# Performance work log

Measured on AMD Instinct MI355X. Metric: run time of the kernel, lower is better.

Reference implementation:

```python
import jax, jax.numpy as jnp
import numpy as np

B, S, D = 2, 2048, 2048
H, HD = 16, 128
ROPE_THETA = 10000.0


def _rope_cos_sin(seq_len, head_dim, dtype=jnp.float32):
    inv_freq = 1.0 / (ROPE_THETA ** (jnp.arange(0, head_dim, 2, dtype=jnp.float32) / head_dim))
    t = jnp.arange(seq_len, dtype=jnp.float32)
    freqs = jnp.outer(t, inv_freq)                     # [S, HD/2]
    emb = jnp.concatenate([freqs, freqs], axis=-1)     # [S, HD]
    return jnp.cos(emb).astype(dtype), jnp.sin(emb).astype(dtype)


def _rotate_half(x):
    x1, x2 = jnp.split(x, 2, axis=-1)
    return jnp.concatenate([-x2, x1], axis=-1)


def _apply_rope(x, cos, sin):
    # x: [B, S, H, HD]; cos/sin: [S, HD] -> broadcast over batch and heads
    c = cos[None, :, None, :]
    s = sin[None, :, None, :]
    return x * c + _rotate_half(x) * s


def setup_inputs() -> dict:
    key = jax.random.key(0)
    ks = jax.random.split(key, 6)
    scale = 1.0 / np.sqrt(D)
    hidden_states = jax.random.normal(ks[0], (B, S, D), dtype=jnp.float32)
    # causal additive mask: 0 on/below diagonal, large negative above
    neg = jnp.finfo(jnp.float32).min
    causal = jnp.where(jnp.tril(jnp.ones((S, S), dtype=bool)), 0.0, neg)
    attention_mask = jnp.broadcast_to(causal[None, None, :, :], (B, 1, S, S)).astype(jnp.float32)
    Wq = jax.random.normal(ks[1], (D, D), dtype=jnp.float32) * scale
    Wk = jax.random.normal(ks[2], (D, D), dtype=jnp.float32) * scale
    Wv = jax.random.normal(ks[3], (D, D), dtype=jnp.float32) * scale
    Wo = jax.random.normal(ks[4], (D, D), dtype=jnp.float32) * scale
    return {"hidden_states": hidden_states, "attention_mask": attention_mask,
            "Wq": Wq, "Wk": Wk, "Wv": Wv, "Wo": Wo}


def reference(hidden_states, attention_mask, Wq, Wk, Wv, Wo):
    b, s, d = hidden_states.shape
    # projections (torch Linear: x @ W^T)
    q = (hidden_states @ Wq.T).reshape(b, s, H, HD)
    k = (hidden_states @ Wk.T).reshape(b, s, H, HD)
    v = (hidden_states @ Wv.T).reshape(b, s, H, HD)
    cos, sin = _rope_cos_sin(s, HD, hidden_states.dtype)
    q = _apply_rope(q, cos, sin)
    k = _apply_rope(k, cos, sin)
    # naive attention, [B, H, S, S] scores materialized as in the original
    scores = jnp.einsum('bqhd,bkhd->bhqk', q, k) / np.sqrt(HD)
    scores = scores + attention_mask
    attn = jax.nn.softmax(scores, axis=-1)
    out = jnp.einsum('bhqk,bkhd->bqhd', attn, v).reshape(b, s, d)
    return out @ Wo.T
```

## Files before the change

### kernel.cpp

```cpp
#include <hip/hip_runtime.h>
#include <hip/hip_bf16.h>

typedef __hip_bfloat16 bf16;
typedef __attribute__((ext_vector_type(8))) short s16x8;
typedef __attribute__((ext_vector_type(4))) float f32x4;
typedef __attribute__((ext_vector_type(16))) float f32x16;

#define MFMA16(a, b, c) __builtin_amdgcn_mfma_f32_16x16x32_bf16(a, b, c, 0, 0, 0)
#define MFMA32(a, b, c) __builtin_amdgcn_mfma_f32_32x32x16_bf16(a, b, c, 0, 0, 0)

#define GLL16(gsrc, ldst)                                                                 \
  __builtin_amdgcn_global_load_lds(                                                       \
      (const __attribute__((address_space(1))) unsigned int*)(gsrc),                      \
      (__attribute__((address_space(3))) unsigned int*)(ldst), 16, 0, 0)

#define VMCNT(n) asm volatile("s_waitcnt vmcnt(" #n ")" ::: "memory")
#define BARRIER() __builtin_amdgcn_s_barrier()

static constexpr int S_LEN = 2048;
static constexpr int D_DIM = 2048;
static constexpr int NY = 6144;

union BF4 { ushort4 u; bf16 b[4]; };

__device__ inline unsigned pack2(float a, float b) {
  union { bf16 h[2]; unsigned u; } x;
  x.h[0] = __float2bfloat16(a);
  x.h[1] = __float2bfloat16(b);
  return x.u;
}

__global__ void convert_all(const float* __restrict__ X, const float* __restrict__ Wq,
                            const float* __restrict__ Wk, const float* __restrict__ Wv,
                            const float* __restrict__ Wo, bf16* __restrict__ Xb,
                            bf16* __restrict__ Wb, bf16* __restrict__ Wob,
                            float* __restrict__ cosT, float* __restrict__ sinT) {
  int gid = blockIdx.x * 256 + threadIdx.x;
  if (gid < 6291456) {
    int i4 = gid * 4;
    const float* src;
    bf16* dst;
    int off;
    if (i4 < 8388608) {
      src = X; dst = Xb; off = i4;
    } else {
      int j = i4 - 8388608;
      int seg = j >> 22;
      off = j & 4194303;
      if (seg == 0) { src = Wq; dst = Wb; }
      else if (seg == 1) { src = Wk; dst = Wb + 4194304; }
      else if (seg == 2) { src = Wv; dst = Wb + 8388608; }
      else { src = Wo; dst = Wob; }
    }
    float4 v = *(const float4*)(src + off);
    BF4 o;
    o.b[0] = __float2bfloat16(v.x);
    o.b[1] = __float2bfloat16(v.y);
    o.b[2] = __float2bfloat16(v.z);
    o.b[3] = __float2bfloat16(v.w);
    *(ushort4*)(dst + off) = o.u;
  } else {
    int t4 = (gid - 6291456) * 4;
    if (t4 < 131072) {
#pragma unroll
      for (int k = 0; k < 4; ++k) {
        int i = t4 + k;
        int d = i & 63, s = i >> 6;
        float inv = powf(10000.0f, -(float)d * (1.0f / 64.0f));
        float ang = (float)s * inv;
        cosT[i] = cosf(ang);
        sinT[i] = sinf(ang);
      }
    }
  }
}

__global__ __launch_bounds__(256) void rope_qk(bf16* __restrict__ Y,
                                               const float* __restrict__ cosT,
                                               const float* __restrict__ sinT) {
  int idx = blockIdx.x * 256 + threadIdx.x;
  int quad = idx & 15;
  int h = (idx >> 4) & 15;
  int m = (idx >> 8) & 4095;
  int g = idx >> 20;
  int s = m & (S_LEN - 1);
  int d0 = quad * 4;
  float sc = g ? 1.0f : 0.08838834764831845f * 1.4426950408889634f;
  bf16* p = Y + (size_t)m * NY + g * D_DIM + h * 128 + d0;
  BF4 lo, hi, olo, ohi;
  lo.u = *(const ushort4*)p;
  hi.u = *(const ushort4*)(p + 64);
  float4 c = *(const float4*)(cosT + s * 64 + d0);
  float4 sn = *(const float4*)(sinT + s * 64 + d0);
  float cc[4] = {c.x, c.y, c.z, c.w};
  float ss[4] = {sn.x, sn.y, sn.z, sn.w};
#pragma unroll
  for (int i = 0; i < 4; ++i) {
    float x1 = __bfloat162float(lo.b[i]);
    float x2 = __bfloat162float(hi.b[i]);
    olo.b[i] = __float2bfloat16((x1 * cc[i] - x2 * ss[i]) * sc);
    ohi.b[i] = __float2bfloat16((x2 * cc[i] + x1 * ss[i]) * sc);
  }
  *(ushort4*)p = olo.u;
  *(ushort4*)(p + 64) = ohi.u;
}

__device__ inline void storeC(float* p, float v) { *p = v; }
__device__ inline void storeC(bf16* p, float v) { *p = __float2bfloat16(v); }

__global__ __launch_bounds__(512, 2) void gemm256(const bf16* __restrict__ A,
                                                  const bf16* __restrict__ Bm,
                                                  bf16* __restrict__ C, int K, int lda,
                                                  int ldb, int ldc, int mt) {
  __shared__ __align__(16) char lds[131072];
  char* A0buf = lds;
  char* B0buf = lds + 32768;
  char* A1buf = lds + 65536;
  char* B1buf = lds + 98304;
  const int tid = threadIdx.x;
  const int lane = tid & 63;
  const int w = tid >> 6;
  const int wm = w >> 2, wn = w & 3;
  const int l15 = lane & 15, lh4 = lane >> 4;
  const int xr = l15 & 7;
  const int xo0 = ((lh4 ^ xr) << 4);
  const int xo1 = (((4 + lh4) ^ xr) << 4);

  const int nwg = gridDim.x;
  const int bid = blockIdx.x;
  const int swz = (bid & 7) * (nwg >> 3) + (bid >> 3);
  const int bm = swz % mt, bn = swz / mt;
  const int row0 = bm * 256, col0 = bn * 256;

  const int srow8 = lane >> 3;
  const int scol = ((lane & 7) ^ srow8) * 8;
  const bf16* gA_s = A + (size_t)(row0 + w * 8 + srow8) * lda + scol;
  const bf16* gB_s = Bm + (size_t)(col0 + (w >> 2) * 64 + (w & 3) * 8 + srow8) * ldb + scol;
  const int ldst = w * 1024;

#define STAGE_A(bufa, rh, k0)                                                     \
  {                                                                               \
    GLL16(gA_s + (size_t)((rh)*64) * lda + (k0), (bufa) + (rh)*16384 + ldst);     \
    GLL16(gA_s + (size_t)((rh)*64 + 128) * lda + (k0),                            \
          (bufa) + (rh)*16384 + 8192 + ldst);                                     \
  }
#define STAGE_B(bufb, ch, k0)                                                     \
  {                                                                               \
    GLL16(gB_s + (size_t)((ch)*32) * ldb + (k0), (bufb) + (ch)*16384 + ldst);     \
    GLL16(gB_s + (size_t)((ch)*32 + 128) * ldb + (k0),                            \
          (bufb) + (ch)*16384 + 8192 + ldst);                                     \
  }

  f32x4 acc[8][4];
#pragma unroll
  for (int i = 0; i < 8; ++i)
#pragma unroll
    for (int j = 0; j < 4; ++j) acc[i][j] = (f32x4){0.f, 0.f, 0.f, 0.f};

  s16x8 af[4][2];
  s16x8 bfr[2][2];

#define READ_AH(bufa, rh)                                                         \
  _Pragma("unroll") for (int ii = 0; ii < 4; ++ii) {                              \
    const char* p_ = (bufa) + (rh)*16384 + (wm * 64 + ii * 16 + l15) * 128;       \
    af[ii][0] = *(const s16x8*)(p_ + xo0);                                        \
    af[ii][1] = *(const s16x8*)(p_ + xo1);                                        \
  }
#define READ_BH(bufb, ch)                                                         \
  _Pragma("unroll") for (int jj = 0; jj < 2; ++jj) {                              \
    const char* p_ = (bufb) + (ch)*16384 + (wn * 32 + jj * 16 + l15) * 128;       \
    bfr[jj][0] = *(const s16x8*)(p_ + xo0);                                       \
    bfr[jj][1] = *(const s16x8*)(p_ + xo1);                                       \
  }
#define QUAD(rh, ch)                                                              \
  __builtin_amdgcn_s_setprio(1);                                                  \
  _Pragma("unroll") for (int jj = 0; jj < 2; ++jj)                                \
  _Pragma("unroll") for (int ii = 0; ii < 4; ++ii)                                \
  _Pragma("unroll") for (int ks = 0; ks < 2; ++ks)                                \
      acc[(rh)*4 + ii][(ch)*2 + jj] =                                             \
          MFMA16(af[ii][ks], bfr[jj][ks], acc[(rh)*4 + ii][(ch)*2 + jj]);         \
  __builtin_amdgcn_s_setprio(0);

  STAGE_A(A0buf, 0, 0);
  STAGE_B(B0buf, 0, 0);
  STAGE_B(B0buf, 1, 0);
  STAGE_A(A0buf, 1, 0);
  STAGE_A(A1buf, 0, 64);
  STAGE_B(B1buf, 1, 64);
  STAGE_A(A1buf, 1, 64);
  VMCNT(6);
  BARRIER();

  const int NI = K >> 7;
  for (int i = 0; i < NI; ++i) {
    const int kT1 = (2 * i + 1) << 6;
    const int kT2 = (2 * i + 2) << 6;
    const int kT3 = (2 * i + 3) << 6;
    const bool nl = (i + 1 < NI);
    READ_AH(A0buf, 0);
    READ_BH(B0buf, 0);
    STAGE_B(B1buf, 0, kT1);
    BARRIER();
    QUAD(0, 0);
    BARRIER();
    READ_BH(B0buf, 1);
    if (nl) STAGE_A(A0buf, 0, kT2);
    BARRIER();
    QUAD(0, 1);
    BARRIER();
    READ_AH(A0buf, 1);
    if (nl) STAGE_B(B0buf, 1, kT2);
    BARRIER();
    QUAD(1, 1);
    BARRIER();
    READ_BH(B0buf, 0);
    if (nl) STAGE_A(A0buf, 1, kT2);
    BARRIER();
    QUAD(1, 0);
    if (nl) { VMCNT(6); } else { VMCNT(0); }
    BARRIER();
    READ_AH(A1buf, 0);
    READ_BH(B1buf, 0);
    if (nl) STAGE_B(B0buf, 0, kT2);
    BARRIER();
    QUAD(0, 0);
    BARRIER();
    READ_BH(B1buf, 1);
    if (nl) STAGE_A(A1buf, 0, kT3);
    BARRIER();
    QUAD(0, 1);
    BARRIER();
    READ_AH(A1buf, 1);
    if (nl) STAGE_B(B1buf, 1, kT3);
    BARRIER();
    QUAD(1, 1);
    BARRIER();
    READ_BH(B1buf, 0);
    if (nl) STAGE_A(A1buf, 1, kT3);
    BARRIER();
    QUAD(1, 0);
    if (nl) { VMCNT(6); }
    BARRIER();
  }
#undef STAGE_A
#undef STAGE_B
#undef READ_AH
#undef READ_BH
#undef QUAD

#pragma unroll
  for (int ri = 0; ri < 8; ++ri)
#pragma unroll
    for (int cj = 0; cj < 4; ++cj) {
      int gr = row0 + wm * 128 + ri * 16 + lh4 * 4;
      int gc = col0 + wn * 64 + cj * 16 + l15;
#pragma unroll
      for (int rr = 0; rr < 4; ++rr)
        C[(size_t)(gr + rr) * ldc + gc] = __float2bfloat16(acc[ri][cj][rr]);
    }
}

template <typename OutT, bool TRANSV>
__global__ __launch_bounds__(512, 2) void gemm_fine(const bf16* __restrict__ A,
                                                    const bf16* __restrict__ Bm,
                                                    OutT* __restrict__ C, int K, int lda,
                                                    int ldb, int ldc, int mt) {
  __shared__ __align__(16) char lds[147456];
  char* b0 = lds;
  char* b1 = lds + 49152;
  char* b2 = lds + 98304;
  const int tid = threadIdx.x;
  const int lane = tid & 63;
  const int w = tid >> 6;
  const int wm = w >> 2, wn = w & 3;
  const int l15 = lane & 15, lh4 = lane >> 4;
  const int xr = l15 & 7;
  const int xo0 = ((lh4 ^ xr) << 4);
  const int xo1 = (((4 + lh4) ^ xr) << 4);

  const int nwg = gridDim.x;
  const int bid = blockIdx.x;
  const int swz = (bid & 7) * (nwg >> 3) + (bid >> 3);
  const int bm = swz % mt, bn = swz / mt;
  const int row0 = bm * 128, col0 = bn * 256;

  const int srow = w * 8 + (lane >> 3);
  const int scol = ((lane & 7) ^ (lane >> 3)) * 8;
  const bf16* gA = A + (size_t)(row0 + srow) * lda + scol;
  const bf16* gB = Bm + (size_t)(col0 + srow) * ldb + scol;
  const int ldst = w * 1024;

  f32x4 acc[4][4];
#pragma unroll
  for (int i = 0; i < 4; ++i)
#pragma unroll
    for (int j = 0; j < 4; ++j) acc[i][j] = (f32x4){0.f, 0.f, 0.f, 0.f};

  s16x8 af[4], bfr[4];

#define PH_READ(BUF, XO)                                                          \
  _Pragma("unroll") for (int ii = 0; ii < 4; ++ii)                                \
      af[ii] = *(const s16x8*)((BUF) + (wm * 64 + ii * 16 + l15) * 128 + (XO));   \
  _Pragma("unroll") for (int jj = 0; jj < 4; ++jj)                                \
      bfr[jj] = *(const s16x8*)((BUF) + 16384 + (wn * 64 + jj * 16 + l15) * 128 + (XO));
#define PH_FMA()                                                                  \
  __builtin_amdgcn_s_setprio(1);                                                  \
  _Pragma("unroll") for (int jj = 0; jj < 4; ++jj)                                \
  _Pragma("unroll") for (int ii = 0; ii < 4; ++ii)                                \
      acc[ii][jj] = MFMA16(af[ii], bfr[jj], acc[ii][jj]);                         \
  __builtin_amdgcn_s_setprio(0);
#define STAGE_T(BUF, kS)                                                          \
  GLL16(gA + (kS), (BUF) + ldst);                                                 \
  GLL16(gA + (size_t)64 * lda + (kS), (BUF) + 8192 + ldst);                       \
  GLL16(gB + (kS), (BUF) + 16384 + ldst);                                         \
  GLL16(gB + (size_t)64 * ldb + (kS), (BUF) + 24576 + ldst);                      \
  GLL16(gB + (size_t)128 * ldb + (kS), (BUF) + 32768 + ldst);                     \
  GLL16(gB + (size_t)192 * ldb + (kS), (BUF) + 40960 + ldst);
#define TILE_MAIN(RBUF, SBUF, kS)                                                 \
  PH_READ(RBUF, xo0);                                                             \
  GLL16(gA + (kS), (SBUF) + ldst);                                                \
  GLL16(gA + (size_t)64 * lda + (kS), (SBUF) + 8192 + ldst);                      \
  GLL16(gB + (kS), (SBUF) + 16384 + ldst);                                        \
  BARRIER();                                                                      \
  PH_FMA();                                                                       \
  BARRIER();                                                                      \
  PH_READ(RBUF, xo1);                                                             \
  GLL16(gB + (size_t)64 * ldb + (kS), (SBUF) + 24576 + ldst);                     \
  GLL16(gB + (size_t)128 * ldb + (kS), (SBUF) + 32768 + ldst);                    \
  GLL16(gB + (size_t)192 * ldb + (kS), (SBUF) + 40960 + ldst);                    \
  BARRIER();                                                                      \
  PH_FMA();                                                                       \
  VMCNT(6);                                                                       \
  BARRIER();

  STAGE_T(b0, 0);
  STAGE_T(b1, 64);
  VMCNT(6);
  BARRIER();

  const int NT = K >> 6;
  for (int t = 0; t < NT - 2; t += 3) {
    TILE_MAIN(b0, b2, (size_t)(t + 2) * 64);
    TILE_MAIN(b1, b0, (size_t)(t + 3) * 64);
    TILE_MAIN(b2, b1, (size_t)(t + 4) * 64);
  }
  PH_READ(b0, xo0);
  BARRIER();
  PH_FMA();
  BARRIER();
  PH_READ(b0, xo1);
  BARRIER();
  PH_FMA();
  VMCNT(0);
  BARRIER();
  PH_READ(b1, xo0);
  BARRIER();
  PH_FMA();
  BARRIER();
  PH_READ(b1, xo1);
  BARRIER();
  PH_FMA();
#undef PH_READ
#undef PH_FMA
#undef STAGE_T
#undef TILE_MAIN

  if constexpr (TRANSV) {
    bf16* Vt = (bf16*)C;
#pragma unroll
    for (int mi = 0; mi < 4; ++mi)
#pragma unroll
      for (int ni = 0; ni < 4; ++ni) {
        int gr = row0 + wm * 64 + mi * 16 + lh4 * 4;
        int gc = col0 + wn * 64 + ni * 16 + l15;
        size_t vrow = (size_t)((gr >> 11) * 2048 + gc);
        BF4 o;
#pragma unroll
        for (int rr = 0; rr < 4; ++rr) o.b[rr] = __float2bfloat16(acc[mi][ni][rr]);
        *(ushort4*)(Vt + vrow * S_LEN + (gr & (S_LEN - 1))) = o.u;
      }
  } else {
#pragma unroll
    for (int mi = 0; mi < 4; ++mi)
#pragma unroll
      for (int ni = 0; ni < 4; ++ni) {
        int gr = row0 + wm * 64 + mi * 16 + lh4 * 4;
        int gc = col0 + wn * 64 + ni * 16 + l15;
#pragma unroll
        for (int rr = 0; rr < 4; ++rr)
          storeC(&C[(size_t)(gr + rr) * ldc + gc], acc[mi][ni][rr]);
      }
  }
}

__global__ __launch_bounds__(256, 2) void attn_fwd(const bf16* __restrict__ Y,
                                                   const bf16* __restrict__ Vt,
                                                   bf16* __restrict__ At) {
  __shared__ __align__(16) char smem[65536];

  const int idx = blockIdx.x;
  const int qt = (idx < 256) ? (15 - (idx >> 5)) : ((idx - 256) >> 5);
  const int bh = idx & 31;
  const int b = bh >> 4, h = bh & 15;
  const int tid = threadIdx.x;
  const int lane = tid & 63;
  const int w = tid >> 6;
  const int l31 = lane & 31;
  const int hi = lane >> 5;
  const int q0w = qt * 128 + w * 32;
  const int q = q0w + l31;

  s16x8 qf[8];
  {
    const bf16* qb = Y + (size_t)(b * S_LEN + q) * NY + h * 128 + hi * 8;
#pragma unroll
    for (int s = 0; s < 8; ++s) qf[s] = *(const s16x8*)(qb + s * 16);
  }

  f32x16 O[4];
#pragma unroll
  for (int d = 0; d < 4; ++d)
#pragma unroll
    for (int e = 0; e < 16; ++e) O[d][e] = 0.f;
  float m_run = -3.0e38f, l_run = 0.f;

  const bf16* Kbase = Y + (size_t)(b * S_LEN) * NY + 2048 + h * 128;
  const bf16* Vbase = Vt + (size_t)bh * 128 * S_LEN;
  const int tmax = 2 * qt + 1;

  const int rk_ = w * 4 + (lane >> 4);
  const int ck_ = lane & 15;
  const int dv_ = w * 8 + (lane >> 3);
  const int cv_ = lane & 7;

#define STAGE_KV(T, BASE)                                                         \
  {                                                                               \
    const int kv0s = (T)*64;                                                      \
    _Pragma("unroll") for (int j = 0; j < 4; ++j) {                               \
      int rk = j * 16 + rk_;                                                      \
      GLL16(Kbase + (size_t)(kv0s + rk) * NY + ((ck_ ^ (rk & 15)) * 8),           \
            (BASE) + (j * 4096 + w * 1024));                                      \
      int dv = j * 32 + dv_;                                                      \
      GLL16(Vbase + (size_t)dv * S_LEN + kv0s + ((cv_ ^ (dv & 7)) * 8),           \
            (BASE) + 16384 + (j * 4096 + w * 1024));                              \
    }                                                                             \
  }

  STAGE_KV(0, smem);

  for (int t = 0; t <= tmax; ++t) {
    const int kv0 = t * 64;
    const char* cur = smem + (t & 1) * 32768;
    BARRIER();
    if (t < tmax) {
      STAGE_KV(t + 1, smem + ((t + 1) & 1) * 32768);
      VMCNT(8);
    } else {
      VMCNT(0);
    }
    BARRIER();
    if (kv0 > q0w + 31) continue;

    float sv[32];
#pragma unroll
    for (int tt = 0; tt < 2; ++tt) {
      f32x16 se, so;
#pragma unroll
      for (int e = 0; e < 16; ++e) { se[e] = 0.f; so[e] = 0.f; }
      const int rk = tt * 32 + l31;
      const char* kr = cur + rk * 256;
      const int xr = (rk & 15) << 4;
      __builtin_amdgcn_s_setprio(1);
#pragma unroll
      for (int s = 0; s < 8; s += 2) {
        s16x8 kf0 = *(const s16x8*)(kr + ((s * 32 + hi * 16) ^ xr));
        se = MFMA32(kf0, qf[s], se);
        s16x8 kf1 = *(const s16x8*)(kr + (((s + 1) * 32 + hi * 16) ^ xr));
        so = MFMA32(kf1, qf[s + 1], so);
      }
      __builtin_amdgcn_s_setprio(0);
#pragma unroll
      for (int e = 0; e < 16; ++e) sv[tt * 16 + e] = se[e] + so[e];
    }

    if (kv0 + 63 > q0w) {
#pragma unroll
      for (int tt = 0; tt < 2; ++tt)
#pragma unroll
        for (int r = 0; r < 16; ++r) {
          int kvr = kv0 + tt * 32 + (r & 3) + 8 * (r >> 2) + 4 * hi;
          if (kvr > q) sv[tt * 16 + r] = -3.0e38f;
        }
    }

    float m8[8];
#pragma unroll
    for (int i = 0; i < 8; ++i)
      m8[i] = fmaxf(fmaxf(sv[i], sv[i + 8]), fmaxf(sv[i + 16], sv[i + 24]));
    float m2a = fmaxf(fmaxf(m8[0], m8[1]), fmaxf(m8[2], m8[3]));
    float m2b = fmaxf(fmaxf(m8[4], m8[5]), fmaxf(m8[6], m8[7]));
    float pmax = fmaxf(fmaxf(m2a, m2b), __shfl_xor(fmaxf(m2a, m2b), 32, 64));

    bool need = pmax > m_run + 11.54f;
    if (__any(need)) {
      float newm = fmaxf(m_run, pmax);
      float ef = exp2f(m_run - newm);
      m_run = newm;
      l_run *= ef;
#pragma unroll
      for (int d = 0; d < 4; ++d)
#pragma unroll
        for (int e = 0; e < 16; ++e) O[d][e] *= ef;
    }

#pragma unroll
    for (int i = 0; i < 32; ++i) sv[i] = exp2f(sv[i] - m_run);
    float s16v[16];
#pragma unroll
    for (int i = 0; i < 16; ++i) s16v[i] = sv[i] + sv[i + 16];
    float s8v[8];
#pragma unroll
    for (int i = 0; i < 8; ++i) s8v[i] = s16v[i] + s16v[i + 8];
    float s4v[4];
#pragma unroll
    for (int i = 0; i < 4; ++i) s4v[i] = s8v[i] + s8v[i + 4];
    float rsum = (s4v[0] + s4v[1]) + (s4v[2] + s4v[3]);
    rsum += __shfl_xor(rsum, 32, 64);
    l_run += rsum;

    unsigned pw[4][4];
#pragma unroll
    for (int tt = 0; tt < 2; ++tt) {
      const int bs = tt * 16;
      unsigned x01 = pack2(sv[bs + 0], sv[bs + 1]);
      unsigned x23 = pack2(sv[bs + 2], sv[bs + 3]);
      unsigned x45 = pack2(sv[bs + 4], sv[bs + 5]);
      unsigned x67 = pack2(sv[bs + 6], sv[bs + 7]);
      unsigned y01 = pack2(sv[bs + 8], sv[bs + 9]);
      unsigned y23 = pack2(sv[bs + 10], sv[bs + 11]);
      unsigned y45 = pack2(sv[bs + 12], sv[bs + 13]);
      unsigned y67 = pack2(sv[bs + 14], sv[bs + 15]);
      asm volatile("v_permlane32_swap_b32 %0, %1" : "+v"(x01), "+v"(x45));
      asm volatile("v_permlane32_swap_b32 %0, %1" : "+v"(x23), "+v"(x67));
      asm volatile("v_permlane32_swap_b32 %0, %1" : "+v"(y01), "+v"(y45));
      asm volatile("v_permlane32_swap_b32 %0, %1" : "+v"(y23), "+v"(y67));
      pw[tt * 2][0] = x01;
      pw[tt * 2][1] = x23;
      pw[tt * 2][2] = x45;
      pw[tt * 2][3] = x67;
      pw[tt * 2 + 1][0] = y01;
      pw[tt * 2 + 1][1] = y23;
      pw[tt * 2 + 1][2] = y45;
      pw[tt * 2 + 1][3] = y67;
    }

#pragma unroll
    for (int dt = 0; dt < 4; ++dt) {
      const int d = dt * 32 + l31;
      const char* vr = cur + 16384 + d * 128;
      const int xv = (d & 7) << 4;
      __builtin_amdgcn_s_setprio(1);
#pragma unroll
      for (int sl = 0; sl < 4; ++sl) {
        s16x8 vf = *(const s16x8*)(vr + ((sl * 32 + hi * 16) ^ xv));
        union { unsigned u[4]; s16x8 v; } pb;
        pb.u[0] = pw[sl][0];
        pb.u[1] = pw[sl][1];
        pb.u[2] = pw[sl][2];
        pb.u[3] = pw[sl][3];
        O[dt] = MFMA32(vf, pb.v, O[dt]);
      }
      __builtin_amdgcn_s_setprio(0);
    }
  }
#undef STAGE_KV

  __syncthreads();
  const float inv = 1.0f / l_run;
  {
    const int orow = w * 32 + l31;
    const int xo = (orow & 15) << 4;
    char* obase = (char*)smem + orow * 256;
#pragma unroll
    for (int dt = 0; dt < 4; ++dt)
#pragma unroll
      for (int r = 0; r < 16; ++r) {
        int d = dt * 32 + (r & 3) + 8 * (r >> 2) + 4 * hi;
        *(bf16*)(obase + ((d * 2) ^ xo)) = __float2bfloat16(O[dt][r] * inv);
      }
  }
  __syncthreads();
  bf16* dst = At + (size_t)(b * S_LEN + qt * 128) * D_DIM + h * 128;
#pragma unroll
  for (int j = 0; j < 8; ++j) {
    int id = j * 256 + tid;
    int rr = id >> 4, cc = id & 15;
    int4 val = *(const int4*)((char*)smem + rr * 256 + ((cc * 16) ^ ((rr & 15) << 4)));
    *(int4*)(dst + (size_t)rr * D_DIM + cc * 8) = val;
  }
}

extern "C" void kernel_launch(void* const* d_in, const int* in_sizes, int n_in,
                              void* d_out, int out_size, void* d_ws, size_t ws_size,
                              hipStream_t stream) {
  const float* X = (const float*)d_in[0];
  const float* Wq = (const float*)d_in[2];
  const float* Wk = (const float*)d_in[3];
  const float* Wv = (const float*)d_in[4];
  const float* Wo = (const float*)d_in[5];
  float* out = (float*)d_out;
  char* ws = (char*)d_ws;

  bf16* Xb = (bf16*)(ws);
  bf16* Wb = (bf16*)(ws + 16777216);
  bf16* Wob = (bf16*)(ws + 41943040);
  bf16* Y = (bf16*)(ws + 50331648);
  bf16* Vt = (bf16*)(ws + 100663296);
  bf16* At = (bf16*)(ws + 117440512);
  float* cosT = (float*)(ws + 134217728);
  float* sinT = (float*)(ws + 134742016);

  convert_all<<<24704, 256, 0, stream>>>(X, Wq, Wk, Wv, Wo, Xb, Wb, Wob, cosT, sinT);

  gemm256<<<256, 512, 0, stream>>>(Xb, Wb, Y, 2048, 2048, 2048, 6144, 16);
  gemm_fine<bf16, true><<<256, 512, 0, stream>>>(Xb, Wb + (size_t)4096 * 2048, Vt,
                                                 2048, 2048, 2048, 2048, 32);
  rope_qk<<<8192, 256, 0, stream>>>(Y, cosT, sinT);
  attn_fwd<<<512, 256, 0, stream>>>(Y, Vt, At);
  gemm_fine<float, false><<<256, 512, 0, stream>>>(At, Wob, out, 2048, 2048, 2048, 2048, 32);
}
```

Measured before the change: 244.2 us.

## Fuse RoPE and Q scaling into the QK projection GEMM epilogue

Removes the separate rope_qk kernel and applies rotary embedding plus the softmax scale on Q inside the QK projection GEMM epilogue. The B-operand row loading is permuted (permc) so that each wave holds both halves (d and d+64) of a head dimension in its accumulators, letting the epilogue rotate pairs in registers. This avoids a full read-modify-write pass over Q and K and one kernel launch. In exchange the epilogue does extra cos/sin table loads per output element, and the store pattern becomes more scattered.

```diff
diff --git a/kernel.cpp b/kernel.cpp
--- a/kernel.cpp
+++ b/kernel.cpp
@@ -75,43 +75,19 @@
   }
 }
 
-__global__ __launch_bounds__(256) void rope_qk(bf16* __restrict__ Y,
-                                               const float* __restrict__ cosT,
-                                               const float* __restrict__ sinT) {
-  int idx = blockIdx.x * 256 + threadIdx.x;
-  int quad = idx & 15;
-  int h = (idx >> 4) & 15;
-  int m = (idx >> 8) & 4095;
-  int g = idx >> 20;
-  int s = m & (S_LEN - 1);
-  int d0 = quad * 4;
-  float sc = g ? 1.0f : 0.08838834764831845f * 1.4426950408889634f;
-  bf16* p = Y + (size_t)m * NY + g * D_DIM + h * 128 + d0;
-  BF4 lo, hi, olo, ohi;
-  lo.u = *(const ushort4*)p;
-  hi.u = *(const ushort4*)(p + 64);
-  float4 c = *(const float4*)(cosT + s * 64 + d0);
-  float4 sn = *(const float4*)(sinT + s * 64 + d0);
-  float cc[4] = {c.x, c.y, c.z, c.w};
-  float ss[4] = {sn.x, sn.y, sn.z, sn.w};
-#pragma unroll
-  for (int i = 0; i < 4; ++i) {
-    float x1 = __bfloat162float(lo.b[i]);
-    float x2 = __bfloat162float(hi.b[i]);
-    olo.b[i] = __float2bfloat16((x1 * cc[i] - x2 * ss[i]) * sc);
-    ohi.b[i] = __float2bfloat16((x2 * cc[i] + x1 * ss[i]) * sc);
-  }
-  *(ushort4*)p = olo.u;
-  *(ushort4*)(p + 64) = ohi.u;
-}
-
 __device__ inline void storeC(float* p, float v) { *p = v; }
 __device__ inline void storeC(bf16* p, float v) { *p = __float2bfloat16(v); }
 
-__global__ __launch_bounds__(512, 2) void gemm256(const bf16* __restrict__ A,
-                                                  const bf16* __restrict__ Bm,
-                                                  bf16* __restrict__ C, int K, int lda,
-                                                  int ldb, int ldc, int mt) {
+__device__ __forceinline__ int permc(int c) {
+  return (c & ~0x60) | ((c & 0x20) << 1) | ((c & 0x40) >> 1);
+}
+
+__global__ __launch_bounds__(512, 2) void gemm256_rope(const bf16* __restrict__ A,
+                                                       const bf16* __restrict__ Bm,
+                                                       bf16* __restrict__ C, int K, int lda,
+                                                       int ldb, int ldc, int mt,
+                                                       const float* __restrict__ cosT,
+                                                       const float* __restrict__ sinT) {
   __shared__ __align__(16) char lds[131072];
   char* A0buf = lds;
   char* B0buf = lds + 32768;
@@ -135,7 +111,17 @@
   const int srow8 = lane >> 3;
   const int scol = ((lane & 7) ^ srow8) * 8;
   const bf16* gA_s = A + (size_t)(row0 + w * 8 + srow8) * lda + scol;
-  const bf16* gB_s = Bm + (size_t)(col0 + (w >> 2) * 64 + (w & 3) * 8 + srow8) * ldb + scol;
+  const int hr0 = w * 8 + srow8;
+  const int t0 = hr0 >> 5, lo5 = hr0 & 31;
+  const bf16* gBp[2][2];
+#pragma unroll
+  for (int ch = 0; ch < 2; ++ch) {
+#pragma unroll
+    for (int r = 0; r < 2; ++r) {
+      int c = (t0 + 2 * r) * 64 + ch * 32 + lo5;
+      gBp[ch][r] = Bm + (size_t)(col0 + permc(c)) * ldb + scol;
+    }
+  }
   const int ldst = w * 1024;
 
 #define STAGE_A(bufa, rh, k0)                                                     \
@@ -146,9 +132,8 @@
   }
 #define STAGE_B(bufb, ch, k0)                                                     \
   {                                                                               \
-    GLL16(gB_s + (size_t)((ch)*32) * ldb + (k0), (bufb) + (ch)*16384 + ldst);     \
-    GLL16(gB_s + (size_t)((ch)*32 + 128) * ldb + (k0),                            \
-          (bufb) + (ch)*16384 + 8192 + ldst);                                     \
+    GLL16(gBp[ch][0] + (k0), (bufb) + (ch)*16384 + ldst);                         \
+    GLL16(gBp[ch][1] + (k0), (bufb) + (ch)*16384 + 8192 + ldst);                  \
   }
 
   f32x4 acc[8][4];
@@ -248,16 +233,27 @@
 #undef READ_BH
 #undef QUAD
 
-#pragma unroll
-  for (int ri = 0; ri < 8; ++ri)
-#pragma unroll
-    for (int cj = 0; cj < 4; ++cj) {
-      int gr = row0 + wm * 128 + ri * 16 + lh4 * 4;
-      int gc = col0 + wn * 64 + cj * 16 + l15;
-#pragma unroll
-      for (int rr = 0; rr < 4; ++rr)
-        C[(size_t)(gr + rr) * ldc + gc] = __float2bfloat16(acc[ri][cj][rr]);
-    }
+  const float qsc = (col0 < 2048) ? 0.12751682f : 1.0f;
+  const int dbase = (wn & 1) * 32 + l15;
+  const int gcbase = col0 + (wn >> 1) * 128 + (wn & 1) * 32 + l15;
+#pragma unroll
+  for (int ri = 0; ri < 8; ++ri) {
+    const int s0r = row0 + wm * 128 + ri * 16 + lh4 * 4;
+#pragma unroll
+    for (int pp = 0; pp < 2; ++pp) {
+      const int d = dbase + pp * 16;
+      const int gclo = gcbase + pp * 16;
+#pragma unroll
+      for (int rr = 0; rr < 4; ++rr) {
+        const int srow = (s0r + rr) & (S_LEN - 1);
+        float cs = cosT[srow * 64 + d];
+        float sn = sinT[srow * 64 + d];
+        float lo = acc[ri][pp][rr], hi = acc[ri][pp + 2][rr];
+        C[(size_t)(s0r + rr) * ldc + gclo] = __float2bfloat16((lo * cs - hi * sn) * qsc);
+        C[(size_t)(s0r + rr) * ldc + gclo + 64] = __float2bfloat16((hi * cs + lo * sn) * qsc);
+      }
+    }
+  }
 }
 
 template <typename OutT, bool TRANSV>
@@ -622,10 +618,9 @@
 
   convert_all<<<24704, 256, 0, stream>>>(X, Wq, Wk, Wv, Wo, Xb, Wb, Wob, cosT, sinT);
 
-  gemm256<<<256, 512, 0, stream>>>(Xb, Wb, Y, 2048, 2048, 2048, 6144, 16);
+  gemm256_rope<<<256, 512, 0, stream>>>(Xb, Wb, Y, 2048, 2048, 2048, 6144, 16, cosT, sinT);
   gemm_fine<bf16, true><<<256, 512, 0, stream>>>(Xb, Wb + (size_t)4096 * 2048, Vt,
                                                  2048, 2048, 2048, 2048, 32);
-  rope_qk<<<8192, 256, 0, stream>>>(Y, cosT, sinT);
   attn_fwd<<<512, 256, 0, stream>>>(Y, Vt, At);
   gemm_fine<float, false><<<256, 512, 0, stream>>>(At, Wob, out, 2048, 2048, 2048, 2048, 32);
 }
```

Result: faster. 237.4 us, median of 2 (-2.8%).
